# Performance work log

Measured on AMD Instinct MI355X. Metric: run time of the kernel, lower is better.

Reference implementation:

```python
import jax, jax.numpy as jnp
import numpy as np

N = 10000
NFEAT = 256
NHEAD = 4


def setup_inputs() -> dict:
    key = jax.random.key(0)
    k1, k2, k3, k4, k5 = jax.random.split(key, 5)
    stdv = 1.0 / (NFEAT ** 0.5)
    return {
        "adj": jax.random.uniform(k1, (N, N), dtype=jnp.float32),
        "features": jax.random.normal(k2, (N, NFEAT), dtype=jnp.float32),
        "W": jax.random.uniform(k3, (NFEAT, NFEAT), jnp.float32, -stdv, stdv),
        "b": jax.random.uniform(k4, (NFEAT,), jnp.float32, -stdv, stdv),
        "a": jax.random.uniform(k5, (NHEAD, NFEAT, 1), jnp.float32, -stdv, stdv),
    }


def reference(adj, features, W, b, a):
    # --- Laplacian build ---
    deg = adj.sum(axis=1)                              # [N]
    # torch: diag(deg)**-0.5 with inf (off-diag zeros & zero-degree) set to 0
    dinv = jnp.where(deg > 0, deg ** -0.5, 0.0)        # [N]
    # per-head attention: softmax over a size-1 last dim (== ones), kept faithful
    scores = jnp.einsum('nf,hfo->hno', features, a)    # [H, N, 1]
    scores = jax.nn.softmax(scores, axis=2)            # size-1 softmax -> ones
    att = scores.mean(axis=0)[:, 0]                    # [N]
    # D_hat @ (A + diag(att) + I) @ D_hat via diagonal broadcasting (same math)
    M = adj + jnp.diag(att + 1.0)                      # [N, N]
    L = dinv[:, None] * M * dinv[None, :]              # [N, N]
    # --- GCN layer ---
    support = features @ W                             # [N, nhid]
    out = L @ support + b                              # [N, nhid]
    return jax.nn.relu(out)                            # dropout: eval mode (no-op)
```

## Files before the change

kernel.cpp:

```cpp
#include <hip/hip_runtime.h>
#include <hip/hip_bf16.h>
#include <stdint.h>

#define NN 10000
#define NF 256
#define NSTEPS 313
#define NSP 8
#define DEPTH 3

typedef float f32x4 __attribute__((ext_vector_type(4)));
typedef __bf16 bf16x8 __attribute__((ext_vector_type(8)));
typedef unsigned short u16;

__device__ __forceinline__ u16 f2bf(float f) {
    __bf16 h = (__bf16)f;
    return __builtin_bit_cast(u16, h);
}

__global__ __launch_bounds__(256) void k_deg(const float* __restrict__ adj,
                                             float* __restrict__ dinv) {
    const int row = blockIdx.x;
    const f32x4* rp = reinterpret_cast<const f32x4*>(adj + (size_t)row * NN);
    float s = 0.f;
    for (int j = threadIdx.x; j < NN / 4; j += 256) {
        f32x4 v = rp[j];
        s += (v[0] + v[1]) + (v[2] + v[3]);
    }
#pragma unroll
    for (int off = 32; off > 0; off >>= 1) s += __shfl_down(s, off, 64);
    __shared__ float red[4];
    const int lane = threadIdx.x & 63, w = threadIdx.x >> 6;
    if (lane == 0) red[w] = s;
    __syncthreads();
    if (threadIdx.x == 0) {
        float deg = (red[0] + red[1]) + (red[2] + red[3]);
        dinv[row] = deg > 0.f ? 1.0f / sqrtf(deg) : 0.0f;
    }
}

__global__ __launch_bounds__(256) void k_support(const float* __restrict__ feat,
                                                 const float* __restrict__ W,
                                                 const float* __restrict__ dinv,
                                                 const float* __restrict__ bias,
                                                 u16* __restrict__ SPT,
                                                 float* __restrict__ selfbuf) {
    const int j0 = blockIdx.x * 64;
    const int c0 = blockIdx.y * 64;
    __shared__ float flds[128][64];
    const int t = threadIdx.x;
    const int rg = t & 15, cg = t >> 4;
    const int sr = t >> 2, sf = (t & 3) * 32;
    float acc[4][4] = {};

    for (int half = 0; half < 2; ++half) {
        __syncthreads();
        const int gj = j0 + sr;
#pragma unroll
        for (int i = 0; i < 8; ++i) {
            f32x4 v = {};
            if (gj < NN)
                v = *reinterpret_cast<const f32x4*>(&feat[(size_t)gj * NF + half * 128 + sf + i * 4]);
#pragma unroll
            for (int u = 0; u < 4; ++u) flds[sf + i * 4 + u][sr] = v[u];
        }
        __syncthreads();
#pragma unroll 4
        for (int f = 0; f < 128; ++f) {
            f32x4 fv = *reinterpret_cast<const f32x4*>(&flds[f][rg * 4]);
            f32x4 wv = *reinterpret_cast<const f32x4*>(&W[(size_t)(half * 128 + f) * NF + c0 + cg * 4]);
#pragma unroll
            for (int r = 0; r < 4; ++r)
#pragma unroll
                for (int c = 0; c < 4; ++c)
                    acc[r][c] = fmaf(fv[r], wv[c], acc[r][c]);
        }
    }

    const int jb = j0 + rg * 4;
    if (jb < NN) {
        const f32x4 bv = *reinterpret_cast<const f32x4*>(&bias[c0 + cg * 4]);
        u16 bits[4][4];
#pragma unroll
        for (int r = 0; r < 4; ++r) {
            const float dv = dinv[jb + r];
            f32x4 init;
#pragma unroll
            for (int c = 0; c < 4; ++c) {
                const float sp = acc[r][c] * dv;
                bits[r][c] = f2bf(sp);
                init[c] = 2.f * dv * sp + bv[c];
            }
            *reinterpret_cast<f32x4*>(&selfbuf[(size_t)(jb + r) * NF + c0 + cg * 4]) = init;
        }
#pragma unroll
        for (int c = 0; c < 4; ++c) {
            ushort4 v; v.x = bits[0][c]; v.y = bits[1][c]; v.z = bits[2][c]; v.w = bits[3][c];
            *reinterpret_cast<ushort4*>(&SPT[(size_t)(c0 + cg * 4 + c) * NN + jb]) = v;
        }
    }
}

__global__ __launch_bounds__(256, 3) void k_gemm(const float* __restrict__ adj,
                                                 const u16* __restrict__ SPT,
                                                 float* __restrict__ P) {
    const int bid = blockIdx.x;
    const int ks = bid & 7, mt = bid >> 3;
    const int m0 = mt * 64;
    const int t = threadIdx.x;
    const int lane = t & 63, w = t >> 6;
    const int n0 = w * 64;
    const int lrow = lane & 15, lk = lane >> 4;

    const int base = NSTEPS / NSP, extra = NSTEPS % NSP;
    const int s0 = ks * base + (ks < extra ? ks : extra);
    const int s1 = s0 + base + (ks < extra ? 1 : 0);

    __shared__ __align__(16) float Abuf[DEPTH][2048];

    auto stage = [&](int d, int s) {
#pragma unroll
        for (int is = 0; is < 2; ++is) {
            const int r = (t >> 3) + is * 32;
            const int g = (t & 7) ^ (r & 7);
            const int row = m0 + r;
            const int kc = s * 32 + g * 4;
            const float* src = (row < NN && kc < NN) ? (adj + (size_t)row * NN + kc) : adj;
            __builtin_amdgcn_global_load_lds(
                (const __attribute__((address_space(1))) void*)src,
                (__attribute__((address_space(3))) void*)&Abuf[d][t * 4 + is * 1024],
                16, 0, 0);
        }
    };

    const u16* bbase = SPT + (size_t)(n0 + lrow) * NN + lk * 8;
    auto loadB = [&](int s, uint4* bq) {
        const int k0 = s * 32;
        const int kb = ((k0 + lk * 8) < NN) ? k0 : 0;
#pragma unroll
        for (int nf = 0; nf < 4; ++nf)
            bq[nf] = *reinterpret_cast<const uint4*>(bbase + (size_t)nf * 16 * NN + kb);
    };

    f32x4 acc[4][4] = {};
    uint4 bc[4], bn[4];

    loadB(s0, bc);
    stage(0, s0);
    if (s0 + 1 < s1) stage(1, s0 + 1);

    int d_cur = 0;
    for (int s = s0; s < s1; ++s) {
        if (s < s1 - 1) asm volatile("s_waitcnt vmcnt(2)" ::: "memory");
        else            asm volatile("s_waitcnt vmcnt(0)" ::: "memory");
        __builtin_amdgcn_s_barrier();

        if (s + 1 < s1) loadB(s + 1, bn);
        const int d_stage = (d_cur + 2 >= DEPTH) ? d_cur + 2 - DEPTH : d_cur + 2;
        if (s + 2 < s1) stage(d_stage, s + 2);

        const int k0 = s * 32;
        const bool kv = (k0 + lk * 8) < NN;
        const float* ab = Abuf[d_cur];
        const bf16x8 zz = (bf16x8)(__bf16)0.0f;
        bf16x8 af[4], bf[4];
#pragma unroll
        for (int fi = 0; fi < 4; ++fi) {
            const int r = fi * 16 + lrow;
            const int sl0 = (lk * 2) ^ (r & 7);
            const int sl1 = (lk * 2 + 1) ^ (r & 7);
            f32x4 x0 = *reinterpret_cast<const f32x4*>(&ab[r * 32 + sl0 * 4]);
            f32x4 x1 = *reinterpret_cast<const f32x4*>(&ab[r * 32 + sl1 * 4]);
            bf16x8 a;
            a[0] = (__bf16)x0[0]; a[1] = (__bf16)x0[1];
            a[2] = (__bf16)x0[2]; a[3] = (__bf16)x0[3];
            a[4] = (__bf16)x1[0]; a[5] = (__bf16)x1[1];
            a[6] = (__bf16)x1[2]; a[7] = (__bf16)x1[3];
            af[fi] = kv ? a : zz;
            bf[fi] = kv ? *reinterpret_cast<const bf16x8*>(&bc[fi]) : zz;
        }
#pragma unroll
        for (int i = 0; i < 4; ++i)
#pragma unroll
            for (int j = 0; j < 4; ++j)
                acc[i][j] = __builtin_amdgcn_mfma_f32_16x16x32_bf16(af[i], bf[j], acc[i][j], 0, 0, 0);

#pragma unroll
        for (int nf = 0; nf < 4; ++nf) bc[nf] = bn[nf];
        d_cur = (d_cur + 1 == DEPTH) ? 0 : d_cur + 1;
    }

    float* Pp = P + (size_t)ks * ((size_t)NN * NF);
#pragma unroll
    for (int i = 0; i < 4; ++i) {
        const int rb = m0 + i * 16 + lk * 4;
#pragma unroll
        for (int r = 0; r < 4; ++r) {
            const int row = rb + r;
            if (row < NN) {
#pragma unroll
                for (int j = 0; j < 4; ++j)
                    Pp[(size_t)row * NF + n0 + j * 16 + lrow] = acc[i][j][r];
            }
        }
    }
}

__global__ __launch_bounds__(256) void k_out(const float* __restrict__ P,
                                             const float* __restrict__ selfbuf,
                                             const float* __restrict__ dinv,
                                             float* __restrict__ out) {
    const size_t e = ((size_t)blockIdx.x * 256 + threadIdx.x) * 4;
    const int row = (int)(e >> 8);
    f32x4 sum = {};
#pragma unroll
    for (int s = 0; s < NSP; ++s)
        sum += *reinterpret_cast<const f32x4*>(&P[(size_t)s * NN * NF + e]);
    const float dv = dinv[row];
    const f32x4 sf = *reinterpret_cast<const f32x4*>(&selfbuf[e]);
    f32x4 o;
#pragma unroll
    for (int c = 0; c < 4; ++c) o[c] = fmaxf(fmaf(dv, sum[c], sf[c]), 0.f);
    *reinterpret_cast<f32x4*>(&out[e]) = o;
}

extern "C" void kernel_launch(void* const* d_in, const int* in_sizes, int n_in,
                              void* d_out, int out_size, void* d_ws, size_t ws_size,
                              hipStream_t stream) {
    const float* adj  = (const float*)d_in[0];
    const float* feat = (const float*)d_in[1];
    const float* W    = (const float*)d_in[2];
    const float* bias = (const float*)d_in[3];

    char* ws = (char*)d_ws;
    const size_t SPT_OFF  = 0;
    const size_t DINV_OFF = 5120000;
    const size_t SELF_OFF = 5160192;
    const size_t P_OFF    = 15400192;
    u16*   SPT     = (u16*)(ws + SPT_OFF);
    float* dinv    = (float*)(ws + DINV_OFF);
    float* selfbuf = (float*)(ws + SELF_OFF);
    float* P       = (float*)(ws + P_OFF);

    k_deg<<<NN, 256, 0, stream>>>(adj, dinv);
    k_support<<<dim3(157, 4), 256, 0, stream>>>(feat, W, dinv, bias, SPT, selfbuf);
    k_gemm<<<157 * NSP, 256, 0, stream>>>(adj, SPT, P);
    k_out<<<2500, 256, 0, stream>>>(P, selfbuf, dinv, (float*)d_out);
}
```

Measured before the change: 308.0 us.

## Fuse degree reduction with bf16 pre-tiling of adjacency for the GEMM

Replaces the per-row degree kernel with a prep kernel that reads adj once, computes partial row sums and writes a swizzled bf16 tiled copy of adj. A small kernel then finishes the degree reduction. The GEMM stages bf16 tiles straight into LDS without in-loop fp32-to-bf16 conversion, which halves its A-operand traffic and LDS usage. The cost is a 200MB extra write and read of the bf16 copy, and occupancy hint changes from 3 to 2.

```diff
diff --git a/kernel.cpp b/kernel.cpp
--- a/kernel.cpp
+++ b/kernel.cpp
@@ -6,7 +6,6 @@
 #define NF 256
 #define NSTEPS 313
 #define NSP 8
-#define DEPTH 3
 
 typedef float f32x4 __attribute__((ext_vector_type(4)));
 typedef __bf16 bf16x8 __attribute__((ext_vector_type(8)));
@@ -17,24 +16,74 @@
     return __builtin_bit_cast(u16, h);
 }
 
-__global__ __launch_bounds__(256) void k_deg(const float* __restrict__ adj,
-                                             float* __restrict__ dinv) {
-    const int row = blockIdx.x;
-    const f32x4* rp = reinterpret_cast<const f32x4*>(adj + (size_t)row * NN);
-    float s = 0.f;
-    for (int j = threadIdx.x; j < NN / 4; j += 256) {
-        f32x4 v = rp[j];
-        s += (v[0] + v[1]) + (v[2] + v[3]);
-    }
-#pragma unroll
-    for (int off = 32; off > 0; off >>= 1) s += __shfl_down(s, off, 64);
-    __shared__ float red[4];
-    const int lane = threadIdx.x & 63, w = threadIdx.x >> 6;
-    if (lane == 0) red[w] = s;
+__device__ __forceinline__ int split_lo(int part) {
+    const int base = NSTEPS / NSP, extra = NSTEPS % NSP;
+    return part * base + (part < extra ? part : extra);
+}
+
+__global__ __launch_bounds__(256) void k_prep(const float* __restrict__ adj,
+                                              u16* __restrict__ AT,
+                                              float* __restrict__ degp) {
+    const int mt = blockIdx.x, kc = blockIdx.y;
+    const int m0 = mt * 64;
+    const int t = threadIdx.x;
+    const int r = t & 63, w = t >> 6;
+    const int row = m0 + r;
+    const bool rowv = row < NN;
+    const float* rowp = adj + (size_t)(rowv ? row : 0) * NN;
+    const int t0 = split_lo(kc), t1 = split_lo(kc + 1);
+    const int swz = (r >> 1) & 3;
+
+    float psum = 0.f;
+    for (int c0 = t0; c0 < t1; c0 += 8) {
+#pragma unroll
+        for (int j = 0; j < 2; ++j) {
+            const int s = c0 + 2 * w + j;
+            if (s < t1) {
+                const int k0 = s * 32;
+                f32x4 v[8];
+#pragma unroll
+                for (int q = 0; q < 8; ++q) {
+                    const int k = k0 + q * 4;
+                    if (rowv && k < NN) v[q] = *reinterpret_cast<const f32x4*>(rowp + k);
+                    else { v[q][0] = 0.f; v[q][1] = 0.f; v[q][2] = 0.f; v[q][3] = 0.f; }
+                }
+                f32x4 ss = v[0];
+#pragma unroll
+                for (int q = 1; q < 8; ++q) ss += v[q];
+                psum += (ss[0] + ss[1]) + (ss[2] + ss[3]);
+
+                u16* tb = AT + (size_t)(mt * NSTEPS + s) * 2048 + r * 32;
+#pragma unroll
+                for (int c = 0; c < 4; ++c) {
+                    bf16x8 o;
+#pragma unroll
+                    for (int e = 0; e < 4; ++e) {
+                        o[e]     = (__bf16)v[2 * c][e];
+                        o[e + 4] = (__bf16)v[2 * c + 1][e];
+                    }
+                    *reinterpret_cast<bf16x8*>(tb + ((c ^ swz) * 8)) = o;
+                }
+            }
+        }
+    }
+
+    __shared__ float red[4][64];
+    red[w][r] = psum;
     __syncthreads();
-    if (threadIdx.x == 0) {
-        float deg = (red[0] + red[1]) + (red[2] + red[3]);
-        dinv[row] = deg > 0.f ? 1.0f / sqrtf(deg) : 0.0f;
+    if (t < 64 && (m0 + t) < NN) {
+        degp[(size_t)kc * NN + m0 + t] = (red[0][t] + red[1][t]) + (red[2][t] + red[3][t]);
+    }
+}
+
+__global__ __launch_bounds__(256) void k_dinv(const float* __restrict__ degp,
+                                              float* __restrict__ dinv) {
+    const int i = blockIdx.x * 256 + threadIdx.x;
+    if (i < NN) {
+        float d = 0.f;
+#pragma unroll
+        for (int kc = 0; kc < NSP; ++kc) d += degp[(size_t)kc * NN + i];
+        dinv[i] = d > 0.f ? 1.0f / sqrtf(d) : 0.0f;
     }
 }
 
@@ -100,7 +149,7 @@
     }
 }
 
-__global__ __launch_bounds__(256, 3) void k_gemm(const float* __restrict__ adj,
+__global__ __launch_bounds__(256, 2) void k_gemm(const u16* __restrict__ AT,
                                                  const u16* __restrict__ SPT,
                                                  float* __restrict__ P) {
     const int bid = blockIdx.x;
@@ -110,31 +159,26 @@
     const int lane = t & 63, w = t >> 6;
     const int n0 = w * 64;
     const int lrow = lane & 15, lk = lane >> 4;
-
-    const int base = NSTEPS / NSP, extra = NSTEPS % NSP;
-    const int s0 = ks * base + (ks < extra ? ks : extra);
-    const int s1 = s0 + base + (ks < extra ? 1 : 0);
-
-    __shared__ __align__(16) float Abuf[DEPTH][2048];
+    const int swz = (lrow >> 1) & 3;
+    const int aslot = (lk ^ swz) * 8;
+
+    const int s0 = split_lo(ks), s1 = split_lo(ks + 1);
+
+    __shared__ __align__(16) u16 Abuf[3][2048];
 
     auto stage = [&](int d, int s) {
-#pragma unroll
-        for (int is = 0; is < 2; ++is) {
-            const int r = (t >> 3) + is * 32;
-            const int g = (t & 7) ^ (r & 7);
-            const int row = m0 + r;
-            const int kc = s * 32 + g * 4;
-            const float* src = (row < NN && kc < NN) ? (adj + (size_t)row * NN + kc) : adj;
-            __builtin_amdgcn_global_load_lds(
-                (const __attribute__((address_space(1))) void*)src,
-                (__attribute__((address_space(3))) void*)&Abuf[d][t * 4 + is * 1024],
-                16, 0, 0);
-        }
+        const int su = (s < s1) ? s : (s1 - 1);
+        const u16* src = AT + (size_t)(mt * NSTEPS + su) * 2048 + t * 8;
+        __builtin_amdgcn_global_load_lds(
+            (const __attribute__((address_space(1))) void*)src,
+            (__attribute__((address_space(3))) void*)&Abuf[d][t * 8],
+            16, 0, 0);
     };
 
     const u16* bbase = SPT + (size_t)(n0 + lrow) * NN + lk * 8;
     auto loadB = [&](int s, uint4* bq) {
-        const int k0 = s * 32;
+        const int su = (s < s1) ? s : (s1 - 1);
+        const int k0 = su * 32;
         const int kb = ((k0 + lk * 8) < NN) ? k0 : 0;
 #pragma unroll
         for (int nf = 0; nf < 4; ++nf)
@@ -144,50 +188,37 @@
     f32x4 acc[4][4] = {};
     uint4 bc[4], bn[4];
 
+    stage(0, s0);
     loadB(s0, bc);
-    stage(0, s0);
-    if (s0 + 1 < s1) stage(1, s0 + 1);
-
-    int d_cur = 0;
+    stage(1, s0 + 1);
+
+    int dcur = 0;
     for (int s = s0; s < s1; ++s) {
-        if (s < s1 - 1) asm volatile("s_waitcnt vmcnt(2)" ::: "memory");
-        else            asm volatile("s_waitcnt vmcnt(0)" ::: "memory");
+        asm volatile("s_waitcnt vmcnt(1)" ::: "memory");
         __builtin_amdgcn_s_barrier();
 
-        if (s + 1 < s1) loadB(s + 1, bn);
-        const int d_stage = (d_cur + 2 >= DEPTH) ? d_cur + 2 - DEPTH : d_cur + 2;
-        if (s + 2 < s1) stage(d_stage, s + 2);
-
-        const int k0 = s * 32;
-        const bool kv = (k0 + lk * 8) < NN;
-        const float* ab = Abuf[d_cur];
+        loadB(s + 1, bn);
+        stage(dcur >= 1 ? dcur - 1 : 2, s + 2);
+
+        const bool kv = (s * 32 + lk * 8) < NN;
         const bf16x8 zz = (bf16x8)(__bf16)0.0f;
-        bf16x8 af[4], bf[4];
+        bf16x8 af[4], bfv[4];
 #pragma unroll
         for (int fi = 0; fi < 4; ++fi) {
-            const int r = fi * 16 + lrow;
-            const int sl0 = (lk * 2) ^ (r & 7);
-            const int sl1 = (lk * 2 + 1) ^ (r & 7);
-            f32x4 x0 = *reinterpret_cast<const f32x4*>(&ab[r * 32 + sl0 * 4]);
-            f32x4 x1 = *reinterpret_cast<const f32x4*>(&ab[r * 32 + sl1 * 4]);
-            bf16x8 a;
-            a[0] = (__bf16)x0[0]; a[1] = (__bf16)x0[1];
-            a[2] = (__bf16)x0[2]; a[3] = (__bf16)x0[3];
-            a[4] = (__bf16)x1[0]; a[5] = (__bf16)x1[1];
-            a[6] = (__bf16)x1[2]; a[7] = (__bf16)x1[3];
-            af[fi] = kv ? a : zz;
-            bf[fi] = kv ? *reinterpret_cast<const bf16x8*>(&bc[fi]) : zz;
+            af[fi] = *reinterpret_cast<const bf16x8*>(&Abuf[dcur][(fi * 16 + lrow) * 32 + aslot]);
+            bfv[fi] = kv ? *reinterpret_cast<const bf16x8*>(&bc[fi]) : zz;
         }
 #pragma unroll
         for (int i = 0; i < 4; ++i)
 #pragma unroll
             for (int j = 0; j < 4; ++j)
-                acc[i][j] = __builtin_amdgcn_mfma_f32_16x16x32_bf16(af[i], bf[j], acc[i][j], 0, 0, 0);
+                acc[i][j] = __builtin_amdgcn_mfma_f32_16x16x32_bf16(af[i], bfv[j], acc[i][j], 0, 0, 0);
 
 #pragma unroll
         for (int nf = 0; nf < 4; ++nf) bc[nf] = bn[nf];
-        d_cur = (d_cur + 1 == DEPTH) ? 0 : d_cur + 1;
-    }
+        dcur = (dcur + 1 == 3) ? 0 : dcur + 1;
+    }
+    asm volatile("s_waitcnt vmcnt(0)" ::: "memory");
 
     float* Pp = P + (size_t)ks * ((size_t)NN * NF);
 #pragma unroll
@@ -232,17 +263,22 @@
     const float* bias = (const float*)d_in[3];
 
     char* ws = (char*)d_ws;
-    const size_t SPT_OFF  = 0;
-    const size_t DINV_OFF = 5120000;
-    const size_t SELF_OFF = 5160192;
-    const size_t P_OFF    = 15400192;
+    const size_t AT_OFF   = 0;
+    const size_t SPT_OFF  = 201281536;
+    const size_t DEGP_OFF = 206401536;
+    const size_t DINV_OFF = 206721536;
+    const size_t SELF_OFF = 206761536;
+    const size_t P_OFF    = 217001536;
+    u16*   AT      = (u16*)(ws + AT_OFF);
     u16*   SPT     = (u16*)(ws + SPT_OFF);
+    float* degp    = (float*)(ws + DEGP_OFF);
     float* dinv    = (float*)(ws + DINV_OFF);
     float* selfbuf = (float*)(ws + SELF_OFF);
     float* P       = (float*)(ws + P_OFF);
 
-    k_deg<<<NN, 256, 0, stream>>>(adj, dinv);
+    k_prep<<<dim3(157, NSP), 256, 0, stream>>>(adj, AT, degp);
+    k_dinv<<<40, 256, 0, stream>>>(degp, dinv);
     k_support<<<dim3(157, 4), 256, 0, stream>>>(feat, W, dinv, bias, SPT, selfbuf);
-    k_gemm<<<157 * NSP, 256, 0, stream>>>(adj, SPT, P);
+    k_gemm<<<157 * NSP, 256, 0, stream>>>(AT, SPT, P);
     k_out<<<2500, 256, 0, stream>>>(P, selfbuf, dinv, (float*)d_out);
 }
```

Result: slower. 419.6 us (+36.2%).

## Stage 256-wide K chunks of adj with double buffering in k_gemm

Applied to the files above, without the earlier changes.

The GEMM kernel now stages 64x256 fp32 tiles of adj into LDS with two buffers instead of 32-wide K steps with triple buffering. This means one barrier and one vmcnt wait per 8 MFMA sub-steps, and each wave loads whole contiguous row segments, so global loads are longer and contiguous. The split-K partition becomes fixed chunks (40 chunks, 5 per split). The cost is 128KB of LDS per block, which limits occupancy to about one block per CU, and the pipeline now drains fully (vmcnt 0) before every chunk.

```diff
diff --git a/kernel.cpp b/kernel.cpp
--- a/kernel.cpp
+++ b/kernel.cpp
@@ -4,9 +4,10 @@
 
 #define NN 10000
 #define NF 256
-#define NSTEPS 313
 #define NSP 8
-#define DEPTH 3
+#define BK 256
+#define NCH 40
+#define CPB 5
 
 typedef float f32x4 __attribute__((ext_vector_type(4)));
 typedef __bf16 bf16x8 __attribute__((ext_vector_type(8)));
@@ -100,9 +101,9 @@
     }
 }
 
-__global__ __launch_bounds__(256, 3) void k_gemm(const float* __restrict__ adj,
-                                                 const u16* __restrict__ SPT,
-                                                 float* __restrict__ P) {
+__global__ __launch_bounds__(256) void k_gemm(const float* __restrict__ adj,
+                                              const u16* __restrict__ SPT,
+                                              float* __restrict__ P) {
     const int bid = blockIdx.x;
     const int ks = bid & 7, mt = bid >> 3;
     const int m0 = mt * 64;
@@ -110,31 +111,33 @@
     const int lane = t & 63, w = t >> 6;
     const int n0 = w * 64;
     const int lrow = lane & 15, lk = lane >> 4;
-
-    const int base = NSTEPS / NSP, extra = NSTEPS % NSP;
-    const int s0 = ks * base + (ks < extra ? ks : extra);
-    const int s1 = s0 + base + (ks < extra ? 1 : 0);
-
-    __shared__ __align__(16) float Abuf[DEPTH][2048];
-
-    auto stage = [&](int d, int s) {
-#pragma unroll
-        for (int is = 0; is < 2; ++is) {
-            const int r = (t >> 3) + is * 32;
-            const int g = (t & 7) ^ (r & 7);
+    const int c0 = ks * CPB;
+
+    __shared__ __align__(16) float Abuf[2][64][BK];
+
+    auto stage = [&](int b, int c) {
+        const int kbase = c * BK;
+        const int gl = (lane & 56) | ((lane & 7) ^ 0);
+#pragma unroll
+        for (int i = 0; i < 16; ++i) {
+            const int r = w * 16 + i;
             const int row = m0 + r;
-            const int kc = s * 32 + g * 4;
-            const float* src = (row < NN && kc < NN) ? (adj + (size_t)row * NN + kc) : adj;
+            const int rc = row < NN ? row : NN - 1;
+            const int g = (lane & 56) | ((lane & 7) ^ (r & 7));
+            int kf = kbase + g * 4;
+            if (kf > NN - 4) kf = NN - 4;
+            const float* src = adj + (size_t)rc * NN + kf;
             __builtin_amdgcn_global_load_lds(
                 (const __attribute__((address_space(1))) void*)src,
-                (__attribute__((address_space(3))) void*)&Abuf[d][t * 4 + is * 1024],
+                (__attribute__((address_space(3))) void*)&Abuf[b][r][lane * 4],
                 16, 0, 0);
         }
+        (void)gl;
     };
 
     const u16* bbase = SPT + (size_t)(n0 + lrow) * NN + lk * 8;
-    auto loadB = [&](int s, uint4* bq) {
-        const int k0 = s * 32;
+    auto loadB = [&](int c, int st, uint4* bq) {
+        const int k0 = c * BK + st * 32;
         const int kb = ((k0 + lk * 8) < NN) ? k0 : 0;
 #pragma unroll
         for (int nf = 0; nf < 4; ++nf)
@@ -143,50 +146,48 @@
 
     f32x4 acc[4][4] = {};
     uint4 bc[4], bn[4];
-
-    loadB(s0, bc);
-    stage(0, s0);
-    if (s0 + 1 < s1) stage(1, s0 + 1);
-
-    int d_cur = 0;
-    for (int s = s0; s < s1; ++s) {
-        if (s < s1 - 1) asm volatile("s_waitcnt vmcnt(2)" ::: "memory");
-        else            asm volatile("s_waitcnt vmcnt(0)" ::: "memory");
+    const bf16x8 zz = (bf16x8)(__bf16)0.0f;
+
+    stage(0, c0);
+    loadB(c0, 0, bc);
+
+    for (int cc = 0; cc < CPB; ++cc) {
+        const int c = c0 + cc;
+        asm volatile("s_waitcnt vmcnt(0)" ::: "memory");
         __builtin_amdgcn_s_barrier();
-
-        if (s + 1 < s1) loadB(s + 1, bn);
-        const int d_stage = (d_cur + 2 >= DEPTH) ? d_cur + 2 - DEPTH : d_cur + 2;
-        if (s + 2 < s1) stage(d_stage, s + 2);
-
-        const int k0 = s * 32;
-        const bool kv = (k0 + lk * 8) < NN;
-        const float* ab = Abuf[d_cur];
-        const bf16x8 zz = (bf16x8)(__bf16)0.0f;
-        bf16x8 af[4], bf[4];
-#pragma unroll
-        for (int fi = 0; fi < 4; ++fi) {
-            const int r = fi * 16 + lrow;
-            const int sl0 = (lk * 2) ^ (r & 7);
-            const int sl1 = (lk * 2 + 1) ^ (r & 7);
-            f32x4 x0 = *reinterpret_cast<const f32x4*>(&ab[r * 32 + sl0 * 4]);
-            f32x4 x1 = *reinterpret_cast<const f32x4*>(&ab[r * 32 + sl1 * 4]);
-            bf16x8 a;
-            a[0] = (__bf16)x0[0]; a[1] = (__bf16)x0[1];
-            a[2] = (__bf16)x0[2]; a[3] = (__bf16)x0[3];
-            a[4] = (__bf16)x1[0]; a[5] = (__bf16)x1[1];
-            a[6] = (__bf16)x1[2]; a[7] = (__bf16)x1[3];
-            af[fi] = kv ? a : zz;
-            bf[fi] = kv ? *reinterpret_cast<const bf16x8*>(&bc[fi]) : zz;
-        }
-#pragma unroll
-        for (int i = 0; i < 4; ++i)
-#pragma unroll
-            for (int j = 0; j < 4; ++j)
-                acc[i][j] = __builtin_amdgcn_mfma_f32_16x16x32_bf16(af[i], bf[j], acc[i][j], 0, 0, 0);
-
-#pragma unroll
-        for (int nf = 0; nf < 4; ++nf) bc[nf] = bn[nf];
-        d_cur = (d_cur + 1 == DEPTH) ? 0 : d_cur + 1;
+        if (cc + 1 < CPB) stage((cc + 1) & 1, c + 1);
+
+        const float* ab = &Abuf[cc & 1][0][0];
+#pragma unroll
+        for (int st = 0; st < 8; ++st) {
+            if (st < 7)            loadB(c, st + 1, bn);
+            else if (cc + 1 < CPB) loadB(c + 1, 0, bn);
+
+            const bool kv = (c * BK + st * 32 + lk * 8) < NN;
+            bf16x8 af[4], bfv[4];
+#pragma unroll
+            for (int fi = 0; fi < 4; ++fi) {
+                const int r = fi * 16 + lrow;
+                const int sl0 = st * 8 + ((lk * 2) ^ (r & 7));
+                const int sl1 = st * 8 + ((lk * 2 + 1) ^ (r & 7));
+                f32x4 x0 = *reinterpret_cast<const f32x4*>(&ab[r * BK + sl0 * 4]);
+                f32x4 x1 = *reinterpret_cast<const f32x4*>(&ab[r * BK + sl1 * 4]);
+                bf16x8 a;
+                a[0] = (__bf16)x0[0]; a[1] = (__bf16)x0[1];
+                a[2] = (__bf16)x0[2]; a[3] = (__bf16)x0[3];
+                a[4] = (__bf16)x1[0]; a[5] = (__bf16)x1[1];
+                a[6] = (__bf16)x1[2]; a[7] = (__bf16)x1[3];
+                af[fi] = kv ? a : zz;
+                bfv[fi] = kv ? *reinterpret_cast<const bf16x8*>(&bc[fi]) : zz;
+            }
+#pragma unroll
+            for (int i = 0; i < 4; ++i)
+#pragma unroll
+                for (int j = 0; j < 4; ++j)
+                    acc[i][j] = __builtin_amdgcn_mfma_f32_16x16x32_bf16(af[i], bfv[j], acc[i][j], 0, 0, 0);
+#pragma unroll
+            for (int nf = 0; nf < 4; ++nf) bc[nf] = bn[nf];
+        }
     }
 
     float* Pp = P + (size_t)ks * ((size_t)NN * NF);
```

Measured after the change: 354.8 us. 1.15x slower.
